# Performance work log

Measured on AMD Instinct MI355X. Metric: run time of the kernel, lower is better.

The kernel has to match this reference:

```python
import jax, jax.numpy as jnp
import numpy as np
import math

D_MODEL = 512
N_HEADS = 8
RADIUS = 0.5
MAX_NEIGHBORS = 32
B, S = 2, 3072


def setup_inputs() -> dict:
    key = jax.random.key(0)
    ks = jax.random.split(key, 12)
    s = 1.0 / math.sqrt(D_MODEL)
    return {
        "x": jax.random.normal(ks[0], (B, S, D_MODEL), jnp.float32),
        "positions": jax.random.normal(ks[1], (B, S, 3), jnp.float32),
        "Wq": jax.random.normal(ks[2], (D_MODEL, D_MODEL), jnp.float32) * s,
        "bq": jnp.zeros((D_MODEL,), jnp.float32),
        "Wk": jax.random.normal(ks[3], (D_MODEL, D_MODEL), jnp.float32) * s,
        "bk": jnp.zeros((D_MODEL,), jnp.float32),
        "Wv": jax.random.normal(ks[4], (D_MODEL, D_MODEL), jnp.float32) * s,
        "bv": jnp.zeros((D_MODEL,), jnp.float32),
        "Wo": jax.random.normal(ks[5], (D_MODEL, D_MODEL), jnp.float32) * s,
        "bo": jnp.zeros((D_MODEL,), jnp.float32),
    }


def _neighbor_mask(positions):
    # positions: (B, S, 3) -> mask: (B, S, S)
    diff = positions[:, :, None, :] - positions[:, None, :, :]  # (B,S,S,3)
    dist = jnp.linalg.norm(diff, axis=-1)                        # (B,S,S)
    radius_mask = (dist < RADIUS).astype(positions.dtype)
    # top-k nearest by argsort (includes self at distance 0)
    nbr_idx = jnp.argsort(dist, axis=-1)[..., :MAX_NEIGHBORS]    # (B,S,K)
    b_idx = jnp.arange(positions.shape[0])[:, None, None]
    r_idx = jnp.arange(positions.shape[1])[None, :, None]
    topk_mask = jnp.zeros_like(dist).at[b_idx, r_idx, nbr_idx].set(1.0)
    return topk_mask * radius_mask


def reference(x, positions, Wq, bq, Wk, bk, Wv, bv, Wo, bo):
    b, s, d = x.shape
    dh = d // N_HEADS
    scale = math.sqrt(dh)

    mask = _neighbor_mask(positions)  # (B,S,S)

    def proj(W, bias):
        return (x @ W + bias).reshape(b, s, N_HEADS, dh).transpose(0, 2, 1, 3)

    Q = proj(Wq, bq)  # (B,H,S,dh)
    K = proj(Wk, bk)
    V = proj(Wv, bv)

    scores = jnp.einsum('bhsd,bhtd->bhst', Q, K) / scale  # (B,H,S,S)
    neg_inf = jnp.asarray(-jnp.inf, scores.dtype)
    scores = jnp.where(mask[:, None, :, :] == 0, neg_inf, scores)
    attn = jax.nn.softmax(scores, axis=-1)
    attn = jnp.nan_to_num(attn, nan=0.0)  # fully-masked rows -> 0
    out = jnp.einsum('bhst,bhtd->bhsd', attn, V)  # (B,H,S,dh)
    out = out.transpose(0, 2, 1, 3).reshape(b, s, d)
    return out @ Wo + bo
```

## Files before the change

### kernel.cpp

```cpp
#include <hip/hip_runtime.h>
#include <math.h>

#define D_MODEL 512
#define N_HEADS 8
#define DH      64
#define S_LEN   3072
#define BATCH   2
#define KMAX    32
#define M_ROWS  6144
#define CAND_CAP 512

#define TOPK_BLOCKS (M_ROWS / 4)
#define CONV_BLOCKS (M_ROWS * D_MODEL / 1024)
#define PACK_BLOCKS 2048

typedef __attribute__((ext_vector_type(8))) short bf16x8;
typedef __attribute__((ext_vector_type(4))) float f32x4;
typedef __attribute__((ext_vector_type(2))) short s16x2;
typedef unsigned long long u64;

__device__ __forceinline__ float b2f(unsigned int u) {
    return __uint_as_float((u & 0xFFFFu) << 16);
}
__device__ __forceinline__ unsigned short f2b(float f) {
    unsigned int u = __float_as_uint(f);
    return (unsigned short)((u + 0x7FFFu + ((u >> 16) & 1u)) >> 16);
}

#if __has_builtin(__builtin_amdgcn_fdot2_f32_bf16)
#define HAS_DOT2 1
__device__ __forceinline__ float dot2bf(unsigned int a, unsigned int b, float c) {
    return __builtin_amdgcn_fdot2_f32_bf16(
        __builtin_bit_cast(s16x2, a), __builtin_bit_cast(s16x2, b), c, false);
}
#else
#define HAS_DOT2 0
__device__ __forceinline__ float dot2bf(unsigned int a, unsigned int b, float c) {
    return c + b2f(a) * b2f(b) + b2f(a >> 16) * b2f(b >> 16);
}
#endif

__global__ __launch_bounds__(256) void prep_kernel(
    const float* __restrict__ x, const float* __restrict__ pos,
    const float* __restrict__ Wq, const float* __restrict__ bq,
    const float* __restrict__ Wk, const float* __restrict__ bk,
    const float* __restrict__ Wv, const float* __restrict__ bv,
    const float* __restrict__ Wo,
    unsigned short* __restrict__ xb, unsigned short* __restrict__ Wt,
    float* __restrict__ bqkv,
    int* __restrict__ nbr_idx, int* __restrict__ nbr_cnt)
{
    const int bid = blockIdx.x;
    const int tid = threadIdx.x;

    if (bid < TOPK_BLOCKS) {
        __shared__ u64 s_keys[4][CAND_CAP];
        __shared__ int s_n[4];
        const int r0 = bid * 4;
        const int b = (r0 >= S_LEN) ? 1 : 0;
        if (tid < 4) s_n[tid] = 0;
        __syncthreads();

        float qx[4], qy[4], qz[4];
        #pragma unroll
        for (int r = 0; r < 4; ++r) {
            qx[r] = pos[(size_t)(r0 + r) * 3 + 0];
            qy[r] = pos[(size_t)(r0 + r) * 3 + 1];
            qz[r] = pos[(size_t)(r0 + r) * 3 + 2];
        }
        const float* pb = pos + (size_t)b * S_LEN * 3;
        #pragma unroll
        for (int i = 0; i < 12; ++i) {
            const int t = tid + i * 256;
            const float x3 = pb[t * 3 + 0], y3 = pb[t * 3 + 1], z3 = pb[t * 3 + 2];
            #pragma unroll
            for (int r = 0; r < 4; ++r) {
                const float dx = qx[r] - x3, dy = qy[r] - y3, dz = qz[r] - z3;
                const float d2 = dx * dx + dy * dy + dz * dz;
                if (d2 < 0.25f) {
                    const int slot = atomicAdd(&s_n[r], 1);
                    if (slot < CAND_CAP)
                        s_keys[r][slot] = ((u64)__float_as_uint(d2) << 32) | (unsigned)t;
                }
            }
        }
        __syncthreads();

        const int rr = tid >> 6, c0 = tid & 63;
        const int n = min(s_n[rr], CAND_CAP);
        for (int c = c0; c < n; c += 64) {
            const u64 k = s_keys[rr][c];
            int rank = 0;
            for (int j = 0; j < n; ++j) rank += (s_keys[rr][j] < k) ? 1 : 0;
            if (rank < KMAX)
                nbr_idx[(size_t)(r0 + rr) * KMAX + rank] = (int)(k & 0xFFFFFFFFu);
        }
        if (c0 == 0) nbr_cnt[r0 + rr] = min(n, KMAX);
    } else if (bid < TOPK_BLOCKS + CONV_BLOCKS) {
        const int i = ((bid - TOPK_BLOCKS) * 256 + tid) * 4;
        const float4 v = *reinterpret_cast<const float4*>(x + i);
        ushort4 o;
        o.x = f2b(v.x); o.y = f2b(v.y); o.z = f2b(v.z); o.w = f2b(v.w);
        *reinterpret_cast<ushort4*>(xb + i) = o;
    } else {
        const int n = bid - TOPK_BLOCKS - CONV_BLOCKS;
        const float* W; int nn;
        if (n < 512)       { W = Wq; nn = n; }
        else if (n < 1024) { W = Wk; nn = n - 512; }
        else if (n < 1536) { W = Wv; nn = n - 1024; }
        else               { W = Wo; nn = n - 1536; }
        for (int k = tid; k < 512; k += 256)
            Wt[(size_t)n * 512 + k] = f2b(W[(size_t)k * 512 + nn]);
        if (tid == 0 && n < 1536) {
            const float* bsel = (n < 512) ? bq : (n < 1024) ? bk : bv;
            bqkv[n] = bsel[nn];
        }
    }
}

template <bool OUT_BF16>
__global__ __launch_bounds__(256) void gemm_mfma_kernel(
    const unsigned short* __restrict__ A,
    const unsigned short* __restrict__ Bt,
    const float* __restrict__ bias,
    void* __restrict__ Cv, int ldc)
{
    constexpr int K = 512;
    __shared__ __align__(16) unsigned short As[128 * 32];
    __shared__ __align__(16) unsigned short Bs[128 * 32];

    const int tid = threadIdx.x;
    const int m0 = blockIdx.x * 128;
    const int n0 = blockIdx.y * 128;
    const int wid = tid >> 6;
    const int lane = tid & 63;
    const int wm = (wid >> 1) * 64;
    const int wn = (wid & 1) * 64;
    const int l15 = lane & 15;
    const int kg = lane >> 4;

    const int srow = tid >> 2;
    const int sk = (tid & 3) * 8;

    f32x4 acc[4][4] = {};

    for (int kt = 0; kt < K; kt += 32) {
        #pragma unroll
        for (int c = 0; c < 2; ++c) {
            const unsigned short* ga = A + (size_t)(m0 + c * 64 + srow) * K + kt + sk;
            __builtin_amdgcn_global_load_lds(
                (const __attribute__((address_space(1))) void*)ga,
                (__attribute__((address_space(3))) void*)(&As[c * 2048 + tid * 8]),
                16, 0, 0);
            const unsigned short* gb = Bt + (size_t)(n0 + c * 64 + srow) * K + kt + sk;
            __builtin_amdgcn_global_load_lds(
                (const __attribute__((address_space(1))) void*)gb,
                (__attribute__((address_space(3))) void*)(&Bs[c * 2048 + tid * 8]),
                16, 0, 0);
        }
        __syncthreads();

        bf16x8 af[4], bfr[4];
        #pragma unroll
        for (int i = 0; i < 4; ++i) {
            af[i]  = *reinterpret_cast<const bf16x8*>(&As[(wm + i * 16 + l15) * 32 + kg * 8]);
            bfr[i] = *reinterpret_cast<const bf16x8*>(&Bs[(wn + i * 16 + l15) * 32 + kg * 8]);
        }
        #pragma unroll
        for (int i = 0; i < 4; ++i)
            #pragma unroll
            for (int j = 0; j < 4; ++j)
                acc[i][j] = __builtin_amdgcn_mfma_f32_16x16x32_bf16(af[i], bfr[j], acc[i][j], 0, 0, 0);
        __syncthreads();
    }

    const int crow = kg * 4;
    #pragma unroll
    for (int i = 0; i < 4; ++i) {
        #pragma unroll
        for (int j = 0; j < 4; ++j) {
            const int col = n0 + wn + j * 16 + l15;
            const float bb = bias[col];
            #pragma unroll
            for (int r = 0; r < 4; ++r) {
                const int row = m0 + wm + i * 16 + crow + r;
                const float v = acc[i][j][r] + bb;
                if (OUT_BF16)
                    ((unsigned short*)Cv)[(size_t)row * ldc + col] = f2b(v);
                else
                    ((float*)Cv)[(size_t)row * ldc + col] = v;
            }
        }
    }
}

__global__ __launch_bounds__(512) void attn_kernel(
    const unsigned short* __restrict__ qkv,
    const int* __restrict__ nbr_idx,
    const int* __restrict__ nbr_cnt,
    unsigned short* __restrict__ ao)
{
    const int row = blockIdx.x;
    const int b = (row >= S_LEN) ? 1 : 0;
    const int tid = threadIdx.x;
    const int h = tid >> 6;
    const int lane = tid & 63;
    const int j = lane & 31;
    const int half = lane >> 5;

    __shared__ unsigned int s_off[KMAX];
    __shared__ unsigned int sQ[N_HEADS][32];

    const int cnt = nbr_cnt[row];

    if (lane < 32) {
        sQ[h][lane] = ((const unsigned int*)(qkv + (size_t)row * 1536 + h * DH))[lane];
    } else {
        const int j2 = lane - 32;
        int t = nbr_idx[(size_t)row * KMAX + j2];
        t = (j2 < cnt) ? t : 0;
        s_off[j2] = (unsigned int)t * 3072u;
    }

    const char* qkvb_ = (const char*)(qkv + (size_t)b * S_LEN * 1536);

    const unsigned int offj = s_off[j];
    const char* krow = qkvb_ + offj + 1024 + h * 128 + half * 64;
    uint4 ku[4];
    #pragma unroll
    for (int c = 0; c < 4; ++c) ku[c] = ((const uint4*)krow)[c];

    const char* vbase_l = qkvb_ + 2048 + h * 128 + lane * 2;
    unsigned int vr[KMAX];
    #pragma unroll
    for (int jj = 0; jj < KMAX; ++jj)
        vr[jj] = *(const unsigned short*)(vbase_l + s_off[jj]);

    const unsigned int* qws = &sQ[h][half * 16];
    unsigned int kw[16];
    #pragma unroll
    for (int c = 0; c < 4; ++c) {
        kw[c * 4 + 0] = ku[c].x; kw[c * 4 + 1] = ku[c].y;
        kw[c * 4 + 2] = ku[c].z; kw[c * 4 + 3] = ku[c].w;
    }
    float partial = 0.f;
    #pragma unroll
    for (int c = 0; c < 16; ++c) partial = dot2bf(kw[c], qws[c], partial);
    partial += __shfl_down(partial, 32, 64);

    const float sc = (half == 0 && j < cnt) ? partial * 0.125f : -INFINITY;
    float mx = sc;
    #pragma unroll
    for (int off = 16; off; off >>= 1) mx = fmaxf(mx, __shfl_xor(mx, off, 64));
    const float p = (half == 0 && j < cnt) ? expf(sc - mx) : 0.f;
    float sum = p;
    #pragma unroll
    for (int off = 16; off; off >>= 1) sum += __shfl_xor(sum, off, 64);
    const float inv = __uint_as_float(
        __builtin_amdgcn_readfirstlane(__float_as_uint(1.f / sum)));

    const float pn = __shfl_xor(p, 1, 64);
    const unsigned int pw = ((unsigned int)f2b(pn) << 16) | f2b(p);

    float o0 = 0.f, o1 = 0.f;
    #pragma unroll
    for (int i = 0; i < 16; i += 2) {
        const unsigned int w0 = __builtin_amdgcn_readlane(pw, 2 * i);
        const unsigned int w1 = __builtin_amdgcn_readlane(pw, 2 * i + 2);
        const unsigned int vp0 = (vr[2 * i + 1] << 16) | vr[2 * i];
        const unsigned int vp1 = (vr[2 * i + 3] << 16) | vr[2 * i + 2];
        o0 = dot2bf(vp0, w0, o0);
        o1 = dot2bf(vp1, w1, o1);
    }
    const float o = (o0 + o1) * inv;
    ao[(size_t)row * D_MODEL + h * DH + lane] = f2b(o);
}

extern "C" void kernel_launch(void* const* d_in, const int* in_sizes, int n_in,
                              void* d_out, int out_size, void* d_ws, size_t ws_size,
                              hipStream_t stream) {
    const float* x   = (const float*)d_in[0];
    const float* pos = (const float*)d_in[1];
    const float* Wq  = (const float*)d_in[2];
    const float* bq  = (const float*)d_in[3];
    const float* Wk  = (const float*)d_in[4];
    const float* bk  = (const float*)d_in[5];
    const float* Wv  = (const float*)d_in[6];
    const float* bv  = (const float*)d_in[7];
    const float* Wo  = (const float*)d_in[8];
    const float* bo  = (const float*)d_in[9];
    float* out = (float*)d_out;

    unsigned short* xb   = (unsigned short*)d_ws;
    unsigned short* Wt   = xb + (size_t)M_ROWS * 512;
    float*          bqkv = (float*)(Wt + (size_t)2048 * 512);
    unsigned short* qkvb = (unsigned short*)(bqkv + 1536);
    unsigned short* aob  = qkvb + (size_t)M_ROWS * 1536;
    int*            nidx = (int*)(aob + (size_t)M_ROWS * 512);
    int*            ncnt = nidx + (size_t)M_ROWS * KMAX;

    prep_kernel<<<TOPK_BLOCKS + CONV_BLOCKS + PACK_BLOCKS, 256, 0, stream>>>(
        x, pos, Wq, bq, Wk, bk, Wv, bv, Wo, xb, Wt, bqkv, nidx, ncnt);

    dim3 g1(M_ROWS / 128, 1536 / 128);
    gemm_mfma_kernel<true><<<g1, 256, 0, stream>>>(xb, Wt, bqkv, qkvb, 1536);

    attn_kernel<<<M_ROWS, 512, 0, stream>>>(qkvb, nidx, ncnt, aob);

    dim3 g2(M_ROWS / 128, 512 / 128);
    gemm_mfma_kernel<false><<<g2, 256, 0, stream>>>(aob, Wt + (size_t)1536 * 512, bo, out, 512);
}
```

Before: 86.71 us.

## Stage neighbor K rows into LDS via async global_load_lds

The attention kernel now copies each neighbor's full 512-wide K row into shared memory with the direct global-to-LDS load instruction, one wave per four neighbors, with fully coalesced 16-byte lanes. Threads then read their K slice from LDS instead of issuing scattered 16-byte global loads. This adds two block barriers and about 33KB of LDS per block, which may lower occupancy. The neighbor index setup also moves to the first 32 threads with the count broadcast through shared memory.

```diff
diff --git a/kernel.cpp b/kernel.cpp
--- a/kernel.cpp
+++ b/kernel.cpp
@@ -28,13 +28,11 @@
 }
 
 #if __has_builtin(__builtin_amdgcn_fdot2_f32_bf16)
-#define HAS_DOT2 1
 __device__ __forceinline__ float dot2bf(unsigned int a, unsigned int b, float c) {
     return __builtin_amdgcn_fdot2_f32_bf16(
         __builtin_bit_cast(s16x2, a), __builtin_bit_cast(s16x2, b), c, false);
 }
 #else
-#define HAS_DOT2 0
 __device__ __forceinline__ float dot2bf(unsigned int a, unsigned int b, float c) {
     return c + b2f(a) * b2f(b) + b2f(a >> 16) * b2f(b >> 16);
 }
@@ -208,27 +206,37 @@
     const int j = lane & 31;
     const int half = lane >> 5;
 
+    __shared__ __align__(16) unsigned short K_lds[KMAX][520];
     __shared__ unsigned int s_off[KMAX];
     __shared__ unsigned int sQ[N_HEADS][32];
-
-    const int cnt = nbr_cnt[row];
-
-    if (lane < 32) {
+    __shared__ int s_cnt;
+
+    if (tid < KMAX) {
+        const int cnt0 = nbr_cnt[row];
+        int t = nbr_idx[(size_t)row * KMAX + tid];
+        t = (tid < cnt0) ? t : 0;
+        s_off[tid] = (unsigned int)t * 3072u;
+        if (tid == 0) s_cnt = cnt0;
+    }
+    if (lane < 32)
         sQ[h][lane] = ((const unsigned int*)(qkv + (size_t)row * 1536 + h * DH))[lane];
-    } else {
-        const int j2 = lane - 32;
-        int t = nbr_idx[(size_t)row * KMAX + j2];
-        t = (j2 < cnt) ? t : 0;
-        s_off[j2] = (unsigned int)t * 3072u;
-    }
-
-    const char* qkvb_ = (const char*)(qkv + (size_t)b * S_LEN * 1536);
-
-    const unsigned int offj = s_off[j];
-    const char* krow = qkvb_ + offj + 1024 + h * 128 + half * 64;
-    uint4 ku[4];
-    #pragma unroll
-    for (int c = 0; c < 4; ++c) ku[c] = ((const uint4*)krow)[c];
+    __syncthreads();
+
+    const int cnt = s_cnt;
+    const char* qkvb_ = (const char*)qkv + (size_t)b * S_LEN * 3072;
+
+    {
+        const int jb = h * 4;
+        #pragma unroll
+        for (int c = 0; c < 4; ++c) {
+            const int jj = jb + c;
+            const char* src = qkvb_ + s_off[jj] + 1024 + lane * 16;
+            __builtin_amdgcn_global_load_lds(
+                (const __attribute__((address_space(1))) void*)src,
+                (__attribute__((address_space(3))) void*)(&K_lds[jj][0]),
+                16, 0, 0);
+        }
+    }
 
     const char* vbase_l = qkvb_ + 2048 + h * 128 + lane * 2;
     unsigned int vr[KMAX];
@@ -236,16 +244,22 @@
     for (int jj = 0; jj < KMAX; ++jj)
         vr[jj] = *(const unsigned short*)(vbase_l + s_off[jj]);
 
+    __syncthreads();
+
+    const uint4* kp = reinterpret_cast<const uint4*>(&K_lds[j][h * 64 + half * 32]);
+    uint4 ku[4];
+    #pragma unroll
+    for (int c = 0; c < 4; ++c) ku[c] = kp[c];
+
     const unsigned int* qws = &sQ[h][half * 16];
-    unsigned int kw[16];
+    float partial = 0.f;
     #pragma unroll
     for (int c = 0; c < 4; ++c) {
-        kw[c * 4 + 0] = ku[c].x; kw[c * 4 + 1] = ku[c].y;
-        kw[c * 4 + 2] = ku[c].z; kw[c * 4 + 3] = ku[c].w;
-    }
-    float partial = 0.f;
-    #pragma unroll
-    for (int c = 0; c < 16; ++c) partial = dot2bf(kw[c], qws[c], partial);
+        partial = dot2bf(ku[c].x, qws[c * 4 + 0], partial);
+        partial = dot2bf(ku[c].y, qws[c * 4 + 1], partial);
+        partial = dot2bf(ku[c].z, qws[c * 4 + 2], partial);
+        partial = dot2bf(ku[c].w, qws[c * 4 + 3], partial);
+    }
     partial += __shfl_down(partial, 32, 64);
 
     const float sc = (half == 0 && j < cnt) ? partial * 0.125f : -INFINITY;
```

Measured after the change: 81.47 us. 6.1% less time.
